# Performance work log

Hardware: AMD Instinct MI355X
Metric: run time of the kernel (lower is better)

Reference implementation:

```python
import jax, jax.numpy as jnp
import numpy as np

E, N, HID, NH = 250000, 50000, 128, 4
HD = HID // NH  # head_dim = 32


def setup_inputs() -> dict:
    key = jax.random.key(0)
    ks = jax.random.split(key, 16)
    f = lambda k, s: jax.random.normal(k, s, dtype=jnp.float32)
    w = lambda k, s: jax.random.normal(k, s, dtype=jnp.float32) * 0.05
    return {
        "edge_attr": f(ks[0], (E, HID)),
        "node_features": f(ks[1], (N, HID)),
        "regime_probs": jax.random.uniform(ks[2], (3,), dtype=jnp.float32),
        # phase_query / phase_key: Linear(hidden+3 -> hidden)
        "Wq": w(ks[3], (HID, HID + 3)), "bq": jnp.zeros((HID,), jnp.float32),
        "Wk": w(ks[4], (HID, HID + 3)), "bk": jnp.zeros((HID,), jnp.float32),
        # phase_value: Linear(hidden -> hidden)
        "Wv": w(ks[5], (HID, HID)), "bv": jnp.zeros((HID,), jnp.float32),
        # nn.MultiheadAttention packed in-projection [3*hid, hid] and out_proj
        "W_in": w(ks[6], (3 * HID, HID)), "b_in": jnp.zeros((3 * HID,), jnp.float32),
        "W_mo": w(ks[7], (HID, HID)), "b_mo": jnp.zeros((HID,), jnp.float32),
        # output_proj
        "Wo": w(ks[8], (HID, HID)), "bo": jnp.zeros((HID,), jnp.float32),
        "edge_index": jax.random.randint(ks[9], (2, E), 0, N, dtype=jnp.int64),
    }


def reference(edge_attr, node_features, regime_probs,
              Wq, bq, Wk, bk, Wv, bv,
              W_in, b_in, W_mo, b_mo, Wo, bo,
              edge_index):
    e = edge_attr.shape[0]
    src = node_features[edge_index[0]]  # [E, HID] gather
    tgt = node_features[edge_index[1]]  # [E, HID] gather
    reg = jnp.broadcast_to(regime_probs, (e, regime_probs.shape[0]))  # [E, 3]

    q = jnp.concatenate([src, reg], axis=1) @ Wq.T + bq  # [E, HID]
    k = jnp.concatenate([tgt, reg], axis=1) @ Wk.T + bk  # [E, HID]
    v = edge_attr @ Wv.T + bv                             # [E, HID]

    # nn.MultiheadAttention with seq_len 1 (batch_first): in-proj, heads, softmax, out-proj
    Wiq, Wik, Wiv = jnp.split(W_in, 3, axis=0)
    biq, bik, biv = jnp.split(b_in, 3)
    q2 = (q @ Wiq.T + biq).reshape(e, NH, HD)
    k2 = (k @ Wik.T + bik).reshape(e, NH, HD)
    v2 = (v @ Wiv.T + biv).reshape(e, NH, HD)

    scale = 1.0 / jnp.sqrt(jnp.float32(HD))
    scores = jnp.sum(q2 * k2, axis=-1, keepdims=True) * scale  # [E, NH, 1]
    probs = jax.nn.softmax(scores, axis=-1)                    # seq-len-1 -> all ones
    att = (probs * v2).reshape(e, HID)                         # == v2 merged
    att = att @ W_mo.T + b_mo                                  # MHA out_proj

    out = att @ Wo.T + bo                                      # output_proj
    return edge_attr + 0.5 * out
```

## Files before the change

kernel.cpp:

```cpp
#include <hip/hip_runtime.h>
#include <hip/hip_bf16.h>

#define HID 128

typedef __attribute__((ext_vector_type(8))) short short8;
typedef __attribute__((ext_vector_type(4))) float f32x4;

static __device__ __forceinline__ short f2bf(float x) {
    __hip_bfloat16 h = __float2bfloat16(x);
    return *reinterpret_cast<short*>(&h);
}

__global__ void prep_stage(const float* __restrict__ A,
                           const float* __restrict__ B,
                           const float* __restrict__ cin,
                           const float* __restrict__ badd,
                           float* __restrict__ Cf,
                           __hip_bfloat16* __restrict__ Mb, int final_stage,
                           float* __restrict__ cout)
{
    __shared__ float arow[HID];
    const int i = blockIdx.x;
    const int j = threadIdx.x;
    arow[j] = A[i * HID + j];
    __syncthreads();

    float s = 0.f;
    #pragma unroll 8
    for (int k = 0; k < HID; ++k) s += arow[k] * B[k * HID + j];

    if (final_stage) {
        float m = ((i == j) ? 1.0f : 0.0f) + 0.5f * s;
        Mb[i * HID + j] = __float2bfloat16(m);
    } else {
        Cf[i * HID + j] = s;
    }

    if (j == 0) {
        float t = 0.f;
        for (int k = 0; k < HID; ++k) t += arow[k] * cin[k];
        t += badd[i];
        cout[i] = final_stage ? 0.5f * t : t;
    }
}

__global__ __launch_bounds__(256) void edge_gemm(
    const float* __restrict__ ea,
    const __hip_bfloat16* __restrict__ Mb,
    const float* __restrict__ cvec,
    float* __restrict__ out,
    int E, int numTiles)
{
    const int lane = threadIdx.x & 63;
    const int wv   = threadIdx.x >> 6;
    const int q    = lane >> 4;
    const int c    = lane & 15;

    short8 bfrag[8][4];
    #pragma unroll
    for (int nt = 0; nt < 8; ++nt) {
        const __hip_bfloat16* bp = Mb + (size_t)(nt * 16 + c) * HID + q * 8;
        #pragma unroll
        for (int kk = 0; kk < 4; ++kk)
            bfrag[nt][kk] = *reinterpret_cast<const short8*>(bp + kk * 32);
    }
    float cv[8];
    #pragma unroll
    for (int nt = 0; nt < 8; ++nt) cv[nt] = cvec[nt * 16 + c];

    const int slot   = blockIdx.x * 4 + wv;
    const int stride = gridDim.x * 4;

    for (int t = slot; t < numTiles; t += stride) {
        const int edge0 = t * 16;

        int rowA = edge0 + c;
        if (rowA > E - 1) rowA = E - 1;
        const float* ap = ea + (size_t)rowA * HID + q * 8;
        short8 afrag[4];
        #pragma unroll
        for (int kk = 0; kk < 4; ++kk) {
            const float4 f0 = *reinterpret_cast<const float4*>(ap + kk * 32);
            const float4 f1 = *reinterpret_cast<const float4*>(ap + kk * 32 + 4);
            short8 a;
            a[0] = f2bf(f0.x); a[1] = f2bf(f0.y); a[2] = f2bf(f0.z); a[3] = f2bf(f0.w);
            a[4] = f2bf(f1.x); a[5] = f2bf(f1.y); a[6] = f2bf(f1.z); a[7] = f2bf(f1.w);
            afrag[kk] = a;
        }

        f32x4 acc[8];
        #pragma unroll
        for (int nt = 0; nt < 8; ++nt) acc[nt] = (f32x4){0.f, 0.f, 0.f, 0.f};

        #pragma unroll
        for (int kk = 0; kk < 4; ++kk) {
            #pragma unroll
            for (int nt = 0; nt < 8; ++nt)
                acc[nt] = __builtin_amdgcn_mfma_f32_16x16x32_bf16(
                    afrag[kk], bfrag[nt][kk], acc[nt], 0, 0, 0);
        }

        #pragma unroll
        for (int r = 0; r < 4; ++r) {
            const int row = edge0 + q * 4 + r;
            if (row < E) {
                float* op = out + (size_t)row * HID + c;
                #pragma unroll
                for (int nt = 0; nt < 8; ++nt)
                    op[nt * 16] = acc[nt][r] + cv[nt];
            }
        }
    }
}

extern "C" void kernel_launch(void* const* d_in, const int* in_sizes, int n_in,
                              void* d_out, int out_size, void* d_ws, size_t ws_size,
                              hipStream_t stream) {
    const float* ea   = (const float*)d_in[0];
    const float* Wv   = (const float*)d_in[7];
    const float* bv   = (const float*)d_in[8];
    const float* W_in = (const float*)d_in[9];
    const float* b_in = (const float*)d_in[10];
    const float* W_mo = (const float*)d_in[11];
    const float* b_mo = (const float*)d_in[12];
    const float* Wo   = (const float*)d_in[13];
    const float* bo   = (const float*)d_in[14];
    const float* Wiv  = W_in + 2 * HID * HID;
    const float* biv  = b_in + 2 * HID;

    char* ws = (char*)d_ws;
    float*          P1 = (float*)(ws);
    float*          P2 = (float*)(ws + 65536);
    __hip_bfloat16* Mb = (__hip_bfloat16*)(ws + 131072);
    float*          c1 = (float*)(ws + 163840);
    float*          c2 = (float*)(ws + 164352);
    float*          cv = (float*)(ws + 164864);

    const int E = in_sizes[0] / HID;
    const int numTiles = (E + 15) / 16;

    prep_stage<<<dim3(HID), dim3(HID), 0, stream>>>(Wiv,  Wv, bv, biv,  P1, nullptr, 0, c1);
    prep_stage<<<dim3(HID), dim3(HID), 0, stream>>>(W_mo, P1, c1, b_mo, P2, nullptr, 0, c2);
    prep_stage<<<dim3(HID), dim3(HID), 0, stream>>>(Wo,   P2, c2, bo,   nullptr, Mb, 1, cv);

    edge_gemm<<<dim3(2048), dim3(256), 0, stream>>>(
        ea, Mb, cv, (float*)d_out, E, numTiles);
}
```

Measured before the change: 307.5 us.

## Split output columns across waves, prefetch next tile, and shorten weight-fold chain

The weight-folding prep drops from three dependent launches to two. Two independent matrix products and the bias chain now run in parallel, followed by a final product. In the edge GEMM each block now covers one 16-edge tile, with each wave computing 32 output columns via a swapped-operand MFMA so results land as contiguous float4 rows. The next tile's edge_attr is register-prefetched during compute, bias is folded into the accumulator init, and results are written with nontemporal vector stores. The trade-off is that each wave redundantly loads and converts the same A tile, with fewer waves per tile stream.

```diff
diff --git a/kernel.cpp b/kernel.cpp
--- a/kernel.cpp
+++ b/kernel.cpp
@@ -11,37 +11,63 @@
     return *reinterpret_cast<short*>(&h);
 }
 
-__global__ void prep_stage(const float* __restrict__ A,
-                           const float* __restrict__ B,
-                           const float* __restrict__ cin,
-                           const float* __restrict__ badd,
-                           float* __restrict__ Cf,
-                           __hip_bfloat16* __restrict__ Mb, int final_stage,
-                           float* __restrict__ cout)
+__global__ void prep_products(const float* __restrict__ Wo,
+                              const float* __restrict__ W_mo,
+                              const float* __restrict__ Wiv,
+                              const float* __restrict__ Wv,
+                              const float* __restrict__ bv,
+                              const float* __restrict__ biv,
+                              const float* __restrict__ b_mo,
+                              const float* __restrict__ bo,
+                              float* __restrict__ Pl,
+                              float* __restrict__ Pr,
+                              float* __restrict__ cv)
 {
-    __shared__ float arow[HID];
-    const int i = blockIdx.x;
     const int j = threadIdx.x;
-    arow[j] = A[i * HID + j];
+    const int b = blockIdx.x;
+    __shared__ float sh[HID];
+
+    if (b < 256) {
+        const float* A = (b < 128) ? Wo   : Wiv;
+        const float* B = (b < 128) ? W_mo : Wv;
+        float*       C = (b < 128) ? Pl   : Pr;
+        const int i = b & 127;
+        sh[j] = A[i * HID + j];
+        __syncthreads();
+        float s = 0.f;
+        #pragma unroll 16
+        for (int k = 0; k < HID; ++k) s += sh[k] * B[k * HID + j];
+        C[i * HID + j] = s;
+    } else {
+        sh[j] = bv[j];
+        __syncthreads();
+        float t = biv[j];
+        #pragma unroll 16
+        for (int k = 0; k < HID; ++k) t += Wiv[j * HID + k] * sh[k];
+        __syncthreads(); sh[j] = t; __syncthreads();
+        t = b_mo[j];
+        #pragma unroll 16
+        for (int k = 0; k < HID; ++k) t += W_mo[j * HID + k] * sh[k];
+        __syncthreads(); sh[j] = t; __syncthreads();
+        t = bo[j];
+        #pragma unroll 16
+        for (int k = 0; k < HID; ++k) t += Wo[j * HID + k] * sh[k];
+        cv[j] = 0.5f * t;
+    }
+}
+
+__global__ void prep_final(const float* __restrict__ Pl,
+                           const float* __restrict__ Pr,
+                           __hip_bfloat16* __restrict__ Mb)
+{
+    const int i = blockIdx.x, j = threadIdx.x;
+    __shared__ float sh[HID];
+    sh[j] = Pl[i * HID + j];
     __syncthreads();
-
     float s = 0.f;
-    #pragma unroll 8
-    for (int k = 0; k < HID; ++k) s += arow[k] * B[k * HID + j];
-
-    if (final_stage) {
-        float m = ((i == j) ? 1.0f : 0.0f) + 0.5f * s;
-        Mb[i * HID + j] = __float2bfloat16(m);
-    } else {
-        Cf[i * HID + j] = s;
-    }
-
-    if (j == 0) {
-        float t = 0.f;
-        for (int k = 0; k < HID; ++k) t += arow[k] * cin[k];
-        t += badd[i];
-        cout[i] = final_stage ? 0.5f * t : t;
-    }
+    #pragma unroll 16
+    for (int k = 0; k < HID; ++k) s += sh[k] * Pr[k * HID + j];
+    Mb[i * HID + j] = __float2bfloat16(((i == j) ? 1.0f : 0.0f) + 0.5f * s);
 }
 
 __global__ __launch_bounds__(256) void edge_gemm(
@@ -51,72 +77,85 @@
     float* __restrict__ out,
     int E, int numTiles)
 {
-    const int lane = threadIdx.x & 63;
-    const int wv   = threadIdx.x >> 6;
-    const int q    = lane >> 4;
-    const int c    = lane & 15;
+    const int lane  = threadIdx.x & 63;
+    const int wv    = threadIdx.x >> 6;
+    const int q     = lane >> 4;
+    const int c     = lane & 15;
+    const int ncol0 = wv * 32;
 
-    short8 bfrag[8][4];
+    short8 Mfrag[2][4];
     #pragma unroll
-    for (int nt = 0; nt < 8; ++nt) {
-        const __hip_bfloat16* bp = Mb + (size_t)(nt * 16 + c) * HID + q * 8;
+    for (int nt = 0; nt < 2; ++nt) {
+        const __hip_bfloat16* mp = Mb + (size_t)(ncol0 + nt * 16 + c) * HID + q * 8;
         #pragma unroll
         for (int kk = 0; kk < 4; ++kk)
-            bfrag[nt][kk] = *reinterpret_cast<const short8*>(bp + kk * 32);
+            Mfrag[nt][kk] = *reinterpret_cast<const short8*>(mp + kk * 32);
     }
-    float cv[8];
+    f32x4 cvp[2];
     #pragma unroll
-    for (int nt = 0; nt < 8; ++nt) cv[nt] = cvec[nt * 16 + c];
+    for (int nt = 0; nt < 2; ++nt)
+        cvp[nt] = *reinterpret_cast<const f32x4*>(cvec + ncol0 + nt * 16 + q * 4);
 
-    const int slot   = blockIdx.x * 4 + wv;
-    const int stride = gridDim.x * 4;
+    int t = blockIdx.x;
+    if (t >= numTiles) return;
 
-    for (int t = slot; t < numTiles; t += stride) {
-        const int edge0 = t * 16;
-
-        int rowA = edge0 + c;
-        if (rowA > E - 1) rowA = E - 1;
-        const float* ap = ea + (size_t)rowA * HID + q * 8;
-        short8 afrag[4];
+    float4 raw[8];
+    {
+        int row = t * 16 + c; if (row > E - 1) row = E - 1;
+        const float* ap = ea + (size_t)row * HID + q * 8;
         #pragma unroll
         for (int kk = 0; kk < 4; ++kk) {
-            const float4 f0 = *reinterpret_cast<const float4*>(ap + kk * 32);
-            const float4 f1 = *reinterpret_cast<const float4*>(ap + kk * 32 + 4);
-            short8 a;
-            a[0] = f2bf(f0.x); a[1] = f2bf(f0.y); a[2] = f2bf(f0.z); a[3] = f2bf(f0.w);
-            a[4] = f2bf(f1.x); a[5] = f2bf(f1.y); a[6] = f2bf(f1.z); a[7] = f2bf(f1.w);
-            afrag[kk] = a;
+            raw[2 * kk]     = *reinterpret_cast<const float4*>(ap + kk * 32);
+            raw[2 * kk + 1] = *reinterpret_cast<const float4*>(ap + kk * 32 + 4);
+        }
+    }
+
+    while (true) {
+        const int edge0 = t * 16;
+        const int tn    = t + gridDim.x;
+
+        short8 bfrag[4];
+        #pragma unroll
+        for (int kk = 0; kk < 4; ++kk) {
+            const float4 f0 = raw[2 * kk], f1 = raw[2 * kk + 1];
+            short8 v;
+            v[0] = f2bf(f0.x); v[1] = f2bf(f0.y); v[2] = f2bf(f0.z); v[3] = f2bf(f0.w);
+            v[4] = f2bf(f1.x); v[5] = f2bf(f1.y); v[6] = f2bf(f1.z); v[7] = f2bf(f1.w);
+            bfrag[kk] = v;
         }
 
-        f32x4 acc[8];
-        #pragma unroll
-        for (int nt = 0; nt < 8; ++nt) acc[nt] = (f32x4){0.f, 0.f, 0.f, 0.f};
+        if (tn < numTiles) {
+            int row = tn * 16 + c; if (row > E - 1) row = E - 1;
+            const float* ap = ea + (size_t)row * HID + q * 8;
+            #pragma unroll
+            for (int kk = 0; kk < 4; ++kk) {
+                raw[2 * kk]     = *reinterpret_cast<const float4*>(ap + kk * 32);
+                raw[2 * kk + 1] = *reinterpret_cast<const float4*>(ap + kk * 32 + 4);
+            }
+        }
 
+        f32x4 acc[2] = { cvp[0], cvp[1] };
         #pragma unroll
         for (int kk = 0; kk < 4; ++kk) {
-            #pragma unroll
-            for (int nt = 0; nt < 8; ++nt)
-                acc[nt] = __builtin_amdgcn_mfma_f32_16x16x32_bf16(
-                    afrag[kk], bfrag[nt][kk], acc[nt], 0, 0, 0);
+            acc[0] = __builtin_amdgcn_mfma_f32_16x16x32_bf16(Mfrag[0][kk], bfrag[kk], acc[0], 0, 0, 0);
+            acc[1] = __builtin_amdgcn_mfma_f32_16x16x32_bf16(Mfrag[1][kk], bfrag[kk], acc[1], 0, 0, 0);
         }
 
-        #pragma unroll
-        for (int r = 0; r < 4; ++r) {
-            const int row = edge0 + q * 4 + r;
-            if (row < E) {
-                float* op = out + (size_t)row * HID + c;
-                #pragma unroll
-                for (int nt = 0; nt < 8; ++nt)
-                    op[nt * 16] = acc[nt][r] + cv[nt];
-            }
+        const int orow = edge0 + c;
+        if (orow < E) {
+            float* op = out + (size_t)orow * HID + ncol0 + q * 4;
+            __builtin_nontemporal_store(acc[0], reinterpret_cast<f32x4*>(op));
+            __builtin_nontemporal_store(acc[1], reinterpret_cast<f32x4*>(op + 16));
         }
+
+        if (tn >= numTiles) break;
+        t = tn;
     }
 }
 
 extern "C" void kernel_launch(void* const* d_in, const int* in_sizes, int n_in,
                               void* d_out, int out_size, void* d_ws, size_t ws_size,
                               hipStream_t stream) {
-    const float* ea   = (const float*)d_in[0];
     const float* Wv   = (const float*)d_in[7];
     const float* bv   = (const float*)d_in[8];
     const float* W_in = (const float*)d_in[9];
@@ -129,20 +168,18 @@
     const float* biv  = b_in + 2 * HID;
 
     char* ws = (char*)d_ws;
-    float*          P1 = (float*)(ws);
-    float*          P2 = (float*)(ws + 65536);
+    float*          Pl = (float*)(ws);
+    float*          Pr = (float*)(ws + 65536);
     __hip_bfloat16* Mb = (__hip_bfloat16*)(ws + 131072);
-    float*          c1 = (float*)(ws + 163840);
-    float*          c2 = (float*)(ws + 164352);
-    float*          cv = (float*)(ws + 164864);
+    float*          cv = (float*)(ws + 163840);
 
     const int E = in_sizes[0] / HID;
     const int numTiles = (E + 15) / 16;
 
-    prep_stage<<<dim3(HID), dim3(HID), 0, stream>>>(Wiv,  Wv, bv, biv,  P1, nullptr, 0, c1);
-    prep_stage<<<dim3(HID), dim3(HID), 0, stream>>>(W_mo, P1, c1, b_mo, P2, nullptr, 0, c2);
-    prep_stage<<<dim3(HID), dim3(HID), 0, stream>>>(Wo,   P2, c2, bo,   nullptr, Mb, 1, cv);
+    prep_products<<<dim3(257), dim3(HID), 0, stream>>>(
+        Wo, W_mo, Wiv, Wv, bv, biv, b_mo, bo, Pl, Pr, cv);
+    prep_final<<<dim3(HID), dim3(HID), 0, stream>>>(Pl, Pr, Mb);
 
-    edge_gemm<<<dim3(2048), dim3(256), 0, stream>>>(
-        ea, Mb, cv, (float*)d_out, E, numTiles);
+    edge_gemm<<<dim3(1024), dim3(256), 0, stream>>>(
+        (const float*)d_in[0], Mb, cv, (float*)d_out, E, numTiles);
 }
```

Measured after the change: 297.9 us. -3.1%, faster.
